# Optimization experiments

Hardware: AMD Instinct MI355X
Metric: run time of the kernel (lower is better)

## Reference

```python
import jax, jax.numpy as jnp
import numpy as np

B = 256            # user batch size
D = 64             # embedding_dim
NR_USERS = 100000
NR_ITEMS = 10000
HID = 32


def _mlp_params(key, in_dim):
    # Keras Dense default: glorot_uniform weights, zero bias
    dims = [in_dim, HID, HID, HID, 1]
    ws, bs = [], []
    for i in range(4):
        key, k = jax.random.split(key)
        lim = np.sqrt(6.0 / (dims[i] + dims[i + 1])).astype(np.float32)
        ws.append(jax.random.uniform(k, (dims[i], dims[i + 1]), jnp.float32, -lim, lim))
        bs.append(jnp.zeros((dims[i + 1],), jnp.float32))
    return ws, bs


def setup_inputs() -> dict:
    key = jax.random.key(0)
    ks = jax.random.split(key, 6)
    users = jax.random.randint(ks[0], (B,), 0, NR_USERS)
    user_emb = jax.random.normal(ks[1], (NR_USERS, D), jnp.float32)
    item_emb = jax.random.normal(ks[2], (NR_ITEMS, D), jnp.float32)
    inp = {"users": users, "user_emb": user_emb, "item_emb": item_emb}
    for name, k, in_dim in (("l", ks[3], 2 * D), ("r", ks[4], 2 * D), ("p", ks[5], D)):
        ws, bs = _mlp_params(k, in_dim)
        for i in range(4):
            inp[f"{name}w{i}"] = ws[i]
            inp[f"{name}b{i}"] = bs[i]
    return inp


def _pair_head(eu, ie, ws, bs):
    # Faithful to: concat([tile(eu),[1,I,1]], tile(ie,[B,1,1])) @ W0 + b0
    # concat @ W0 == eu @ W0[:D] + ie @ W0[D:]  (avoids materializing [B,I,2D])
    h = jax.nn.relu((eu @ ws[0][:D])[:, None, :] + (ie @ ws[0][D:])[None, :, :] + bs[0])
    h = jax.nn.relu(h @ ws[1] + bs[1])
    h = jax.nn.relu(h @ ws[2] + bs[2])
    return jax.nn.sigmoid(h @ ws[3] + bs[3])[..., 0]  # [B, I]


def _item_head(x, ws, bs):
    h = jax.nn.relu(x @ ws[0] + bs[0])
    h = jax.nn.relu(h @ ws[1] + bs[1])
    h = jax.nn.relu(h @ ws[2] + bs[2])
    return jax.nn.sigmoid(h @ ws[3] + bs[3])[..., 0]  # [I]


def reference(users, user_emb, item_emb,
              lw0, lb0, lw1, lb1, lw2, lb2, lw3, lb3,
              rw0, rb0, rw1, rb1, rw2, rb2, rw3, rb3,
              pw0, pb0, pw1, pb1, pw2, pb2, pw3, pb3):
    eu = user_emb[users]  # [B, D]
    likes = _pair_head(eu, item_emb, [lw0, lw1, lw2, lw3], [lb0, lb1, lb2, lb3])
    rated = _pair_head(eu, item_emb, [rw0, rw1, rw2, rw3], [rb0, rb1, rb2, rb3])
    popular = _item_head(item_emb, [pw0, pw1, pw2, pw3], [pb0, pb1, pb2, pb3])
    # tf.keras.losses.cosine_similarity returns NEGATIVE cosine similarity,
    # so sim = (1 + (-cos)) / 2 = (1 - cos) / 2
    n = eu * jax.lax.rsqrt(jnp.maximum(jnp.sum(eu * eu, -1, keepdims=True), 1e-12))
    cos = n @ n.T  # [B, B]
    user_sim = (1.0 - cos) / 2.0
    return likes, user_sim, rated, popular
```

## Files before the change

### kernel.cpp

```cpp
#include <hip/hip_runtime.h>
#include <hip/hip_bf16.h>

#define NB 256
#define D 64
#define NI 10000

typedef __attribute__((ext_vector_type(8))) short bf16x8;
typedef __attribute__((ext_vector_type(16))) float f32x16;

union PK8 { unsigned u[4]; bf16x8 v; };
union F16Q { f32x16 v; float4 q[4]; };

static constexpr int WS_AL  = 0;
static constexpr int WS_AR  = 8192;
static constexpr int WS_N   = 16384;
static constexpr int WS_CL  = 32768;
static constexpr int WS_CR  = 352768;
static constexpr int WS_TAB = 672768;

static constexpr long OUT_LIKES = 0;
static constexpr long OUT_SIM   = 2560000;
static constexpr long OUT_RATED = 2625536;
static constexpr long OUT_POP   = 5185536;

__device__ __forceinline__ unsigned pkbf(float a, float b) {
    unsigned r;
    asm("v_cvt_pk_bf16_f32 %0, %1, %2" : "=v"(r) : "v"(a), "v"(b));
    return r;
}
__device__ __forceinline__ float relu(float x) { return fmaxf(x, 0.f); }

struct A4 { float4 a0, a1, a2, a3; };
__device__ __forceinline__ A4 ldA(const float* p) {
    A4 r;
    r.a0 = *(const float4*)p;        r.a1 = *(const float4*)(p + 4);
    r.a2 = *(const float4*)(p + 16); r.a3 = *(const float4*)(p + 20);
    return r;
}

__global__ __launch_bounds__(256) void k_prep(
        const int* __restrict__ users, const float* __restrict__ uemb,
        const float* __restrict__ iemb,
        const float* __restrict__ lw0, const float* __restrict__ lb0,
        const float* __restrict__ rw0, const float* __restrict__ rb0,
        const float* __restrict__ lw1, const float* __restrict__ lb1,
        const float* __restrict__ lw2, const float* __restrict__ lb2,
        const float* __restrict__ lw3, const float* __restrict__ lb3,
        const float* __restrict__ rw1, const float* __restrict__ rb1,
        const float* __restrict__ rw2, const float* __restrict__ rb2,
        const float* __restrict__ rw3, const float* __restrict__ rb3,
        const float* __restrict__ pw0, const float* __restrict__ pb0,
        const float* __restrict__ pw1, const float* __restrict__ pb1,
        const float* __restrict__ pw2, const float* __restrict__ pb2,
        const float* __restrict__ pw3, const float* __restrict__ pb3,
        float* __restrict__ ws, float* __restrict__ out) {
    int bx = blockIdx.x, t = threadIdx.x;
    if (bx == 0) {
        if (t >= 128) return;
        int head = t >> 6, lane = t & 63;
        int pr = lane & 31, hi = lane >> 5;
        const float* W1 = head ? rw1 : lw1; const float* B1 = head ? rb1 : lb1;
        const float* W2 = head ? rw2 : lw2; const float* B2 = head ? rb2 : lb2;
        const float* w3 = head ? rw3 : lw3; const float* b3 = head ? rb3 : lb3;
        PK8 w1a, w1b, w2a, w2b, w3a, w3b;
        #pragma unroll
        for (int j = 0; j < 4; ++j) {
            int k0 = 8 * hi + 2 * j;
            w1a.u[j] = pkbf(W1[k0 * 32 + pr],        W1[(k0 + 1) * 32 + pr]);
            w1b.u[j] = pkbf(W1[(16 + k0) * 32 + pr], W1[(17 + k0) * 32 + pr]);
            int fa = ((2 * j) & 3) + 8 * ((2 * j) >> 2) + 4 * hi;
            int fb = ((2 * j + 1) & 3) + 8 * ((2 * j + 1) >> 2) + 4 * hi;
            w2a.u[j] = pkbf(W2[fa * 32 + pr],        W2[fb * 32 + pr]);
            w2b.u[j] = pkbf(W2[(fa + 16) * 32 + pr], W2[(fb + 16) * 32 + pr]);
            w3a.u[j] = pkbf(w3[fa],                  w3[fb]);
            w3b.u[j] = pkbf(w3[fa + 16],             w3[fb + 16]);
        }
        float* base = ws + WS_TAB + head * 4608;
        ((uint4*)base)[0 * 64 + lane] = *(uint4*)&w1a;
        ((uint4*)base)[1 * 64 + lane] = *(uint4*)&w1b;
        ((uint4*)base)[2 * 64 + lane] = *(uint4*)&w2a;
        ((uint4*)base)[3 * 64 + lane] = *(uint4*)&w2b;
        ((uint4*)base)[4 * 64 + lane] = *(uint4*)&w3a;
        ((uint4*)base)[5 * 64 + lane] = *(uint4*)&w3b;
        #pragma unroll
        for (int q = 0; q < 4; ++q) {
            float4 v1, v2;
            #pragma unroll
            for (int e = 0; e < 4; ++e) {
                int r = 4 * q + e;
                int f = (r & 3) + 8 * (r >> 2) + 4 * hi;
                ((float*)&v1)[e] = B1[f];
                ((float*)&v2)[e] = B2[f];
            }
            ((float4*)base)[(6 + q) * 64 + lane]  = v1;
            ((float4*)base)[(10 + q) * 64 + lane] = v2;
        }
        float b3v = b3[0];
        float4 bs; bs.x = b3v; bs.y = b3v; bs.z = b3v; bs.w = b3v;
        #pragma unroll
        for (int q = 0; q < 4; ++q) ((float4*)base)[(14 + q) * 64 + lane] = bs;
    } else if (bx < 80) {
        int wv = t >> 6, lane = t & 63;
        int w = (bx - 1) * 4 + wv;
        if (w >= 313) return;
        int i0 = w * 32;
        int pr = lane & 31, hi = lane >> 5;
        int crow = i0 + pr; if (crow > NI - 1) crow = NI - 1;
        const float4* xr = (const float4*)(iemb + (long)crow * D);
        PK8 xm[4], w0f[4];
        #pragma unroll
        for (int m = 0; m < 4; ++m) {
            float4 xa = xr[4 * m + 2 * hi];
            float4 xb = xr[4 * m + 2 * hi + 1];
            xm[m].u[0] = pkbf(xa.x, xa.y); xm[m].u[1] = pkbf(xa.z, xa.w);
            xm[m].u[2] = pkbf(xb.x, xb.y); xm[m].u[3] = pkbf(xb.z, xb.w);
            #pragma unroll
            for (int j = 0; j < 4; ++j) {
                int r0 = 16 * m + 8 * hi + 2 * j;
                w0f[m].u[j] = pkbf(pw0[r0 * 32 + pr], pw0[(r0 + 1) * 32 + pr]);
            }
        }
        PK8 w1a, w1b, w2a, w2b, w3a, w3b;
        f32x16 b0i, b1i, b2i, b3i;
        #pragma unroll
        for (int j = 0; j < 4; ++j) {
            int fa = ((2 * j) & 3) + 8 * ((2 * j) >> 2) + 4 * hi;
            int fb = ((2 * j + 1) & 3) + 8 * ((2 * j + 1) >> 2) + 4 * hi;
            w1a.u[j] = pkbf(pw1[fa * 32 + pr],        pw1[fb * 32 + pr]);
            w1b.u[j] = pkbf(pw1[(fa + 16) * 32 + pr], pw1[(fb + 16) * 32 + pr]);
            w2a.u[j] = pkbf(pw2[fa * 32 + pr],        pw2[fb * 32 + pr]);
            w2b.u[j] = pkbf(pw2[(fa + 16) * 32 + pr], pw2[(fb + 16) * 32 + pr]);
            w3a.u[j] = pkbf(pw3[fa],                  pw3[fb]);
            w3b.u[j] = pkbf(pw3[fa + 16],             pw3[fb + 16]);
        }
        float b3s = pb3[0];
        #pragma unroll
        for (int r = 0; r < 16; ++r) {
            int f = (r & 3) + 8 * (r >> 2) + 4 * hi;
            b0i[r] = pb0[f]; b1i[r] = pb1[f]; b2i[r] = pb2[f]; b3i[r] = b3s;
        }
        f32x16 acc = b0i;
        acc = __builtin_amdgcn_mfma_f32_32x32x16_bf16(w0f[0].v, xm[0].v, acc, 0, 0, 0);
        acc = __builtin_amdgcn_mfma_f32_32x32x16_bf16(w0f[1].v, xm[1].v, acc, 0, 0, 0);
        acc = __builtin_amdgcn_mfma_f32_32x32x16_bf16(w0f[2].v, xm[2].v, acc, 0, 0, 0);
        acc = __builtin_amdgcn_mfma_f32_32x32x16_bf16(w0f[3].v, xm[3].v, acc, 0, 0, 0);
        PK8 g0, g1;
        #pragma unroll
        for (int j = 0; j < 4; ++j) {
            g0.u[j] = pkbf(relu(acc[2 * j]),     relu(acc[2 * j + 1]));
            g1.u[j] = pkbf(relu(acc[8 + 2 * j]), relu(acc[9 + 2 * j]));
        }
        f32x16 a1 = b1i;
        a1 = __builtin_amdgcn_mfma_f32_32x32x16_bf16(w1a.v, g0.v, a1, 0, 0, 0);
        a1 = __builtin_amdgcn_mfma_f32_32x32x16_bf16(w1b.v, g1.v, a1, 0, 0, 0);
        #pragma unroll
        for (int j = 0; j < 4; ++j) {
            g0.u[j] = pkbf(relu(a1[2 * j]),     relu(a1[2 * j + 1]));
            g1.u[j] = pkbf(relu(a1[8 + 2 * j]), relu(a1[9 + 2 * j]));
        }
        f32x16 a2 = b2i;
        a2 = __builtin_amdgcn_mfma_f32_32x32x16_bf16(w2a.v, g0.v, a2, 0, 0, 0);
        a2 = __builtin_amdgcn_mfma_f32_32x32x16_bf16(w2b.v, g1.v, a2, 0, 0, 0);
        #pragma unroll
        for (int j = 0; j < 4; ++j) {
            g0.u[j] = pkbf(relu(a2[2 * j]),     relu(a2[2 * j + 1]));
            g1.u[j] = pkbf(relu(a2[8 + 2 * j]), relu(a2[9 + 2 * j]));
        }
        f32x16 a3 = b3i;
        a3 = __builtin_amdgcn_mfma_f32_32x32x16_bf16(w3a.v, g0.v, a3, 0, 0, 0);
        a3 = __builtin_amdgcn_mfma_f32_32x32x16_bf16(w3b.v, g1.v, a3, 0, 0, 0);
        float o = 1.f / (1.f + __expf(-a3[0]));
        if (hi == 0 && i0 + pr < NI) out[OUT_POP + i0 + pr] = o;
    } else if (bx < 80 + 1250) {
        int i0 = (bx - 80) * 8;
        __shared__ float xs[8][D];
        for (int idx = t; idx < 8 * D; idx += 256) {
            int it = idx >> 6, d = idx & 63; int gi = i0 + it;
            xs[it][d] = (gi < NI) ? iemb[(long)gi * D + d] : 0.f;
        }
        __syncthreads();
        int it = t >> 5, j = t & 31; int gi = i0 + it;
        float al = 0.f, ar = 0.f;
        #pragma unroll
        for (int d = 0; d < D; ++d) {
            float x = xs[it][d];
            al += x * lw0[(D + d) * 32 + j];
            ar += x * rw0[(D + d) * 32 + j];
        }
        if (gi < NI) { ws[WS_CL + gi * 32 + j] = al; ws[WS_CR + gi * 32 + j] = ar; }
    } else {
        __shared__ float es[4][D];
        int ug = t >> 6, tt = t & 63;
        int b = (bx - 1330) * 4 + ug;
        int u = users[b];
        float e = uemb[(long)u * D + tt];
        float s = e * e;
        #pragma unroll
        for (int off = 32; off; off >>= 1) s += __shfl_down(s, off);
        s = __shfl(s, 0);
        ws[WS_N + b * D + tt] = e * rsqrtf(fmaxf(s, 1e-12f));
        es[ug][tt] = e;
        __syncthreads();
        const float* W0 = (tt < 32) ? lw0 : rw0;
        const float* bb = (tt < 32) ? lb0 : rb0;
        int j = tt & 31;
        float acc = bb[j];
        #pragma unroll
        for (int d = 0; d < D; ++d) acc += es[ug][d] * W0[d * 32 + j];
        ws[((tt < 32) ? WS_AL : WS_AR) + b * 32 + j] = acc;
    }
}

__global__ __launch_bounds__(256, 4) void k_main(
        const float* __restrict__ ws, float* __restrict__ out) {
    __shared__ float tabf[4608];
    int bx = blockIdx.x, t = threadIdx.x;
    if (bx < 2504) {
        int head = bx & 1;
        int ug = (bx >> 1) & 3;
        int ib = bx >> 3;
        int i0 = ib * 32;
        int a_off = head ? WS_AR : WS_AL;
        int c_off = head ? WS_CR : WS_CL;
        float* ob = out + (head ? OUT_RATED : OUT_LIKES);

        {
            const float4* g = (const float4*)(ws + WS_TAB + head * 4608);
            float4* l = (float4*)tabf;
            for (int idx = t; idx < 1152; idx += 256) l[idx] = g[idx];
        }
        __syncthreads();

        int lane = t & 63, wv = t >> 6;
        int pr = lane & 31, hi = lane >> 5;
        int u0 = ug * 64 + wv * 16;

        const uint4*  tu = (const uint4*)tabf;
        const float4* tq = (const float4*)tabf;
        PK8 w1a, w1b, w2a, w2b, w3a, w3b;
        *(uint4*)&w1a = tu[0 * 64 + lane];
        *(uint4*)&w1b = tu[1 * 64 + lane];
        *(uint4*)&w2a = tu[2 * 64 + lane];
        *(uint4*)&w2b = tu[3 * 64 + lane];
        *(uint4*)&w3a = tu[4 * 64 + lane];
        *(uint4*)&w3b = tu[5 * 64 + lane];

        int crow = i0 + pr; if (crow > NI - 1) crow = NI - 1;
        const float* cp = ws + c_off + (long)crow * 32 + 8 * hi;
        float4 c0 = *(const float4*)cp;
        float4 c1 = *(const float4*)(cp + 4);
        float4 c2 = *(const float4*)(cp + 16);
        float4 c3 = *(const float4*)(cp + 20);

        bool valid = (hi == 0) && (i0 + pr < NI);
        float* op = ob + (long)u0 * NI + i0 + pr;
        const float* ap = ws + a_off + 8 * hi + (long)u0 * 32;

        A4 a = ldA(ap);
        for (int u = 0; u < 16; ++u) {
            A4 an = a;
            if (u < 15) an = ldA(ap + (long)(u + 1) * 32);
            PK8 x0, x1;
            x0.u[0] = pkbf(relu(a.a0.x + c0.x), relu(a.a0.y + c0.y));
            x0.u[1] = pkbf(relu(a.a0.z + c0.z), relu(a.a0.w + c0.w));
            x0.u[2] = pkbf(relu(a.a1.x + c1.x), relu(a.a1.y + c1.y));
            x0.u[3] = pkbf(relu(a.a1.z + c1.z), relu(a.a1.w + c1.w));
            x1.u[0] = pkbf(relu(a.a2.x + c2.x), relu(a.a2.y + c2.y));
            x1.u[1] = pkbf(relu(a.a2.z + c2.z), relu(a.a2.w + c2.w));
            x1.u[2] = pkbf(relu(a.a3.x + c3.x), relu(a.a3.y + c3.y));
            x1.u[3] = pkbf(relu(a.a3.z + c3.z), relu(a.a3.w + c3.w));
            F16Q acc;
            acc.q[0] = tq[6 * 64 + lane]; acc.q[1] = tq[7 * 64 + lane];
            acc.q[2] = tq[8 * 64 + lane]; acc.q[3] = tq[9 * 64 + lane];
            acc.v = __builtin_amdgcn_mfma_f32_32x32x16_bf16(w1a.v, x0.v, acc.v, 0, 0, 0);
            acc.v = __builtin_amdgcn_mfma_f32_32x32x16_bf16(w1b.v, x1.v, acc.v, 0, 0, 0);
            PK8 h0, h1;
            #pragma unroll
            for (int j = 0; j < 4; ++j) {
                h0.u[j] = pkbf(relu(acc.v[2 * j]),     relu(acc.v[2 * j + 1]));
                h1.u[j] = pkbf(relu(acc.v[8 + 2 * j]), relu(acc.v[9 + 2 * j]));
            }
            F16Q acc2;
            acc2.q[0] = tq[10 * 64 + lane]; acc2.q[1] = tq[11 * 64 + lane];
            acc2.q[2] = tq[12 * 64 + lane]; acc2.q[3] = tq[13 * 64 + lane];
            acc2.v = __builtin_amdgcn_mfma_f32_32x32x16_bf16(w2a.v, h0.v, acc2.v, 0, 0, 0);
            acc2.v = __builtin_amdgcn_mfma_f32_32x32x16_bf16(w2b.v, h1.v, acc2.v, 0, 0, 0);
            PK8 g0, g1;
            #pragma unroll
            for (int j = 0; j < 4; ++j) {
                g0.u[j] = pkbf(relu(acc2.v[2 * j]),     relu(acc2.v[2 * j + 1]));
                g1.u[j] = pkbf(relu(acc2.v[8 + 2 * j]), relu(acc2.v[9 + 2 * j]));
            }
            F16Q acc3;
            acc3.q[0] = tq[14 * 64 + lane]; acc3.q[1] = tq[15 * 64 + lane];
            acc3.q[2] = tq[16 * 64 + lane]; acc3.q[3] = tq[17 * 64 + lane];
            acc3.v = __builtin_amdgcn_mfma_f32_32x32x16_bf16(w3a.v, g0.v, acc3.v, 0, 0, 0);
            acc3.v = __builtin_amdgcn_mfma_f32_32x32x16_bf16(w3b.v, g1.v, acc3.v, 0, 0, 0);
            float o = 1.f / (1.f + __expf(-acc3.v[0]));
            if (valid) *op = o;
            op += NI;
            a = an;
        }
    } else {
        int b = bx - 2504;
        if (t < D) tabf[t] = ws[WS_N + b * D + t];
        __syncthreads();
        const float4* nj = (const float4*)(ws + WS_N + t * D);
        float acc = 0.f;
        #pragma unroll
        for (int d4 = 0; d4 < 16; ++d4) {
            float4 v = nj[d4];
            acc += tabf[4*d4+0] * v.x + tabf[4*d4+1] * v.y
                 + tabf[4*d4+2] * v.z + tabf[4*d4+3] * v.w;
        }
        out[OUT_SIM + (long)b * 256 + t] = (1.f - acc) * 0.5f;
    }
}

extern "C" void kernel_launch(void* const* d_in, const int* in_sizes, int n_in,
                              void* d_out, int out_size, void* d_ws, size_t ws_size,
                              hipStream_t stream) {
    const int*   users = (const int*)d_in[0];
    const float* uemb  = (const float*)d_in[1];
    const float* iemb  = (const float*)d_in[2];
    const float *lw0 = (const float*)d_in[3],  *lb0 = (const float*)d_in[4];
    const float *lw1 = (const float*)d_in[5],  *lb1 = (const float*)d_in[6];
    const float *lw2 = (const float*)d_in[7],  *lb2 = (const float*)d_in[8];
    const float *lw3 = (const float*)d_in[9],  *lb3 = (const float*)d_in[10];
    const float *rw0 = (const float*)d_in[11], *rb0 = (const float*)d_in[12];
    const float *rw1 = (const float*)d_in[13], *rb1 = (const float*)d_in[14];
    const float *rw2 = (const float*)d_in[15], *rb2 = (const float*)d_in[16];
    const float *rw3 = (const float*)d_in[17], *rb3 = (const float*)d_in[18];
    const float *pw0 = (const float*)d_in[19], *pb0 = (const float*)d_in[20];
    const float *pw1 = (const float*)d_in[21], *pb1 = (const float*)d_in[22];
    const float *pw2 = (const float*)d_in[23], *pb2 = (const float*)d_in[24];
    const float *pw3 = (const float*)d_in[25], *pb3 = (const float*)d_in[26];
    float* ws = (float*)d_ws;
    float* out = (float*)d_out;

    k_prep<<<1394, 256, 0, stream>>>(users, uemb, iemb,
                                     lw0, lb0, rw0, rb0,
                                     lw1, lb1, lw2, lb2, lw3, lb3,
                                     rw1, rb1, rw2, rb2, rw3, rb3,
                                     pw0, pb0, pw1, pb1, pw2, pb2, pw3, pb3,
                                     ws, out);
    k_main<<<2760, 256, 0, stream>>>(ws, out);
}
```

Baseline: 69.26 us.

## Use single-wave blocks in k_main, load weight tables from global, hoist bias tiles

k_main now runs one 64-thread wave per block instead of four waves sharing an LDS copy of the weight/bias table. Each wave reads the table straight from global memory (L2-resident), which removes the LDS staging and the __syncthreads barrier. The per-iteration bias-accumulator LDS reloads are hoisted into registers outside the loop. The cosine-similarity blocks are also split four ways per row, and the explicit prefetch of the next A row is dropped. The costs are redundant global table reads across four times as many blocks, higher register pressure, and the loss of software prefetching.

```diff
diff --git a/kernel.cpp b/kernel.cpp
--- a/kernel.cpp
+++ b/kernel.cpp
@@ -139,8 +139,8 @@
             int f = (r & 3) + 8 * (r >> 2) + 4 * hi;
             b0i[r] = pb0[f]; b1i[r] = pb1[f]; b2i[r] = pb2[f]; b3i[r] = b3s;
         }
-        f32x16 acc = b0i;
-        acc = __builtin_amdgcn_mfma_f32_32x32x16_bf16(w0f[0].v, xm[0].v, acc, 0, 0, 0);
+        f32x16 acc;
+        acc = __builtin_amdgcn_mfma_f32_32x32x16_bf16(w0f[0].v, xm[0].v, b0i, 0, 0, 0);
         acc = __builtin_amdgcn_mfma_f32_32x32x16_bf16(w0f[1].v, xm[1].v, acc, 0, 0, 0);
         acc = __builtin_amdgcn_mfma_f32_32x32x16_bf16(w0f[2].v, xm[2].v, acc, 0, 0, 0);
         acc = __builtin_amdgcn_mfma_f32_32x32x16_bf16(w0f[3].v, xm[3].v, acc, 0, 0, 0);
@@ -150,24 +150,24 @@
             g0.u[j] = pkbf(relu(acc[2 * j]),     relu(acc[2 * j + 1]));
             g1.u[j] = pkbf(relu(acc[8 + 2 * j]), relu(acc[9 + 2 * j]));
         }
-        f32x16 a1 = b1i;
-        a1 = __builtin_amdgcn_mfma_f32_32x32x16_bf16(w1a.v, g0.v, a1, 0, 0, 0);
+        f32x16 a1;
+        a1 = __builtin_amdgcn_mfma_f32_32x32x16_bf16(w1a.v, g0.v, b1i, 0, 0, 0);
         a1 = __builtin_amdgcn_mfma_f32_32x32x16_bf16(w1b.v, g1.v, a1, 0, 0, 0);
         #pragma unroll
         for (int j = 0; j < 4; ++j) {
             g0.u[j] = pkbf(relu(a1[2 * j]),     relu(a1[2 * j + 1]));
             g1.u[j] = pkbf(relu(a1[8 + 2 * j]), relu(a1[9 + 2 * j]));
         }
-        f32x16 a2 = b2i;
-        a2 = __builtin_amdgcn_mfma_f32_32x32x16_bf16(w2a.v, g0.v, a2, 0, 0, 0);
+        f32x16 a2;
+        a2 = __builtin_amdgcn_mfma_f32_32x32x16_bf16(w2a.v, g0.v, b2i, 0, 0, 0);
         a2 = __builtin_amdgcn_mfma_f32_32x32x16_bf16(w2b.v, g1.v, a2, 0, 0, 0);
         #pragma unroll
         for (int j = 0; j < 4; ++j) {
             g0.u[j] = pkbf(relu(a2[2 * j]),     relu(a2[2 * j + 1]));
             g1.u[j] = pkbf(relu(a2[8 + 2 * j]), relu(a2[9 + 2 * j]));
         }
-        f32x16 a3 = b3i;
-        a3 = __builtin_amdgcn_mfma_f32_32x32x16_bf16(w3a.v, g0.v, a3, 0, 0, 0);
+        f32x16 a3;
+        a3 = __builtin_amdgcn_mfma_f32_32x32x16_bf16(w3a.v, g0.v, b3i, 0, 0, 0);
         a3 = __builtin_amdgcn_mfma_f32_32x32x16_bf16(w3b.v, g1.v, a3, 0, 0, 0);
         float o = 1.f / (1.f + __expf(-a3[0]));
         if (hi == 0 && i0 + pr < NI) out[OUT_POP + i0 + pr] = o;
@@ -211,32 +211,23 @@
     }
 }
 
-__global__ __launch_bounds__(256, 4) void k_main(
+__global__ __launch_bounds__(64, 4) void k_main(
         const float* __restrict__ ws, float* __restrict__ out) {
-    __shared__ float tabf[4608];
-    int bx = blockIdx.x, t = threadIdx.x;
-    if (bx < 2504) {
+    int bx = blockIdx.x, lane = threadIdx.x;
+    if (bx < 10016) {
         int head = bx & 1;
-        int ug = (bx >> 1) & 3;
-        int ib = bx >> 3;
+        int ug = (bx >> 1) & 15;
+        int ib = bx >> 5;
         int i0 = ib * 32;
         int a_off = head ? WS_AR : WS_AL;
         int c_off = head ? WS_CR : WS_CL;
         float* ob = out + (head ? OUT_RATED : OUT_LIKES);
 
-        {
-            const float4* g = (const float4*)(ws + WS_TAB + head * 4608);
-            float4* l = (float4*)tabf;
-            for (int idx = t; idx < 1152; idx += 256) l[idx] = g[idx];
-        }
-        __syncthreads();
-
-        int lane = t & 63, wv = t >> 6;
         int pr = lane & 31, hi = lane >> 5;
-        int u0 = ug * 64 + wv * 16;
-
-        const uint4*  tu = (const uint4*)tabf;
-        const float4* tq = (const float4*)tabf;
+        int u0 = ug * 16;
+
+        const uint4*  tu = (const uint4*)(ws + WS_TAB + head * 4608);
+        const float4* tq = (const float4*)(ws + WS_TAB + head * 4608);
         PK8 w1a, w1b, w2a, w2b, w3a, w3b;
         *(uint4*)&w1a = tu[0 * 64 + lane];
         *(uint4*)&w1b = tu[1 * 64 + lane];
@@ -244,6 +235,13 @@
         *(uint4*)&w2b = tu[3 * 64 + lane];
         *(uint4*)&w3a = tu[4 * 64 + lane];
         *(uint4*)&w3b = tu[5 * 64 + lane];
+        F16Q bin1, bin2, bin3;
+        bin1.q[0] = tq[6 * 64 + lane];  bin1.q[1] = tq[7 * 64 + lane];
+        bin1.q[2] = tq[8 * 64 + lane];  bin1.q[3] = tq[9 * 64 + lane];
+        bin2.q[0] = tq[10 * 64 + lane]; bin2.q[1] = tq[11 * 64 + lane];
+        bin2.q[2] = tq[12 * 64 + lane]; bin2.q[3] = tq[13 * 64 + lane];
+        bin3.q[0] = tq[14 * 64 + lane]; bin3.q[1] = tq[15 * 64 + lane];
+        bin3.q[2] = tq[16 * 64 + lane]; bin3.q[3] = tq[17 * 64 + lane];
 
         int crow = i0 + pr; if (crow > NI - 1) crow = NI - 1;
         const float* cp = ws + c_off + (long)crow * 32 + 8 * hi;
@@ -256,23 +254,20 @@
         float* op = ob + (long)u0 * NI + i0 + pr;
         const float* ap = ws + a_off + 8 * hi + (long)u0 * 32;
 
-        A4 a = ldA(ap);
         for (int u = 0; u < 16; ++u) {
-            A4 an = a;
-            if (u < 15) an = ldA(ap + (long)(u + 1) * 32);
+            A4 a = ldA(ap + (long)u * 32);
+            float4 s0 = a.a0 + c0, s1 = a.a1 + c1, s2 = a.a2 + c2, s3 = a.a3 + c3;
             PK8 x0, x1;
-            x0.u[0] = pkbf(relu(a.a0.x + c0.x), relu(a.a0.y + c0.y));
-            x0.u[1] = pkbf(relu(a.a0.z + c0.z), relu(a.a0.w + c0.w));
-            x0.u[2] = pkbf(relu(a.a1.x + c1.x), relu(a.a1.y + c1.y));
-            x0.u[3] = pkbf(relu(a.a1.z + c1.z), relu(a.a1.w + c1.w));
-            x1.u[0] = pkbf(relu(a.a2.x + c2.x), relu(a.a2.y + c2.y));
-            x1.u[1] = pkbf(relu(a.a2.z + c2.z), relu(a.a2.w + c2.w));
-            x1.u[2] = pkbf(relu(a.a3.x + c3.x), relu(a.a3.y + c3.y));
-            x1.u[3] = pkbf(relu(a.a3.z + c3.z), relu(a.a3.w + c3.w));
+            x0.u[0] = pkbf(relu(s0.x), relu(s0.y));
+            x0.u[1] = pkbf(relu(s0.z), relu(s0.w));
+            x0.u[2] = pkbf(relu(s1.x), relu(s1.y));
+            x0.u[3] = pkbf(relu(s1.z), relu(s1.w));
+            x1.u[0] = pkbf(relu(s2.x), relu(s2.y));
+            x1.u[1] = pkbf(relu(s2.z), relu(s2.w));
+            x1.u[2] = pkbf(relu(s3.x), relu(s3.y));
+            x1.u[3] = pkbf(relu(s3.z), relu(s3.w));
             F16Q acc;
-            acc.q[0] = tq[6 * 64 + lane]; acc.q[1] = tq[7 * 64 + lane];
-            acc.q[2] = tq[8 * 64 + lane]; acc.q[3] = tq[9 * 64 + lane];
-            acc.v = __builtin_amdgcn_mfma_f32_32x32x16_bf16(w1a.v, x0.v, acc.v, 0, 0, 0);
+            acc.v = __builtin_amdgcn_mfma_f32_32x32x16_bf16(w1a.v, x0.v, bin1.v, 0, 0, 0);
             acc.v = __builtin_amdgcn_mfma_f32_32x32x16_bf16(w1b.v, x1.v, acc.v, 0, 0, 0);
             PK8 h0, h1;
             #pragma unroll
@@ -281,9 +276,7 @@
                 h1.u[j] = pkbf(relu(acc.v[8 + 2 * j]), relu(acc.v[9 + 2 * j]));
             }
             F16Q acc2;
-            acc2.q[0] = tq[10 * 64 + lane]; acc2.q[1] = tq[11 * 64 + lane];
-            acc2.q[2] = tq[12 * 64 + lane]; acc2.q[3] = tq[13 * 64 + lane];
-            acc2.v = __builtin_amdgcn_mfma_f32_32x32x16_bf16(w2a.v, h0.v, acc2.v, 0, 0, 0);
+            acc2.v = __builtin_amdgcn_mfma_f32_32x32x16_bf16(w2a.v, h0.v, bin2.v, 0, 0, 0);
             acc2.v = __builtin_amdgcn_mfma_f32_32x32x16_bf16(w2b.v, h1.v, acc2.v, 0, 0, 0);
             PK8 g0, g1;
             #pragma unroll
@@ -292,28 +285,25 @@
                 g1.u[j] = pkbf(relu(acc2.v[8 + 2 * j]), relu(acc2.v[9 + 2 * j]));
             }
             F16Q acc3;
-            acc3.q[0] = tq[14 * 64 + lane]; acc3.q[1] = tq[15 * 64 + lane];
-            acc3.q[2] = tq[16 * 64 + lane]; acc3.q[3] = tq[17 * 64 + lane];
-            acc3.v = __builtin_amdgcn_mfma_f32_32x32x16_bf16(w3a.v, g0.v, acc3.v, 0, 0, 0);
+            acc3.v = __builtin_amdgcn_mfma_f32_32x32x16_bf16(w3a.v, g0.v, bin3.v, 0, 0, 0);
             acc3.v = __builtin_amdgcn_mfma_f32_32x32x16_bf16(w3b.v, g1.v, acc3.v, 0, 0, 0);
             float o = 1.f / (1.f + __expf(-acc3.v[0]));
             if (valid) *op = o;
             op += NI;
-            a = an;
         }
     } else {
-        int b = bx - 2504;
-        if (t < D) tabf[t] = ws[WS_N + b * D + t];
-        __syncthreads();
-        const float4* nj = (const float4*)(ws + WS_N + t * D);
+        int bs = bx - 10016;
+        int b = bs >> 2, j = (bs & 3) * 64 + lane;
+        const float4* nb = (const float4*)(ws + WS_N + b * D);
+        const float4* nj = (const float4*)(ws + WS_N + j * D);
         float acc = 0.f;
         #pragma unroll
         for (int d4 = 0; d4 < 16; ++d4) {
+            float4 u = nb[d4];
             float4 v = nj[d4];
-            acc += tabf[4*d4+0] * v.x + tabf[4*d4+1] * v.y
-                 + tabf[4*d4+2] * v.z + tabf[4*d4+3] * v.w;
-        }
-        out[OUT_SIM + (long)b * 256 + t] = (1.f - acc) * 0.5f;
+            acc += u.x * v.x + u.y * v.y + u.z * v.z + u.w * v.w;
+        }
+        out[OUT_SIM + (long)b * 256 + j] = (1.f - acc) * 0.5f;
     }
 }
 
@@ -344,5 +334,5 @@
                                      rw1, rb1, rw2, rb2, rw3, rb3,
                                      pw0, pb0, pw1, pb1, pw2, pb2, pw3, pb3,
                                      ws, out);
-    k_main<<<2760, 256, 0, stream>>>(ws, out);
-}
+    k_main<<<11040, 64, 0, stream>>>(ws, out);
+}
```

Result: no change. 68.64 us (-0.9%).
